# Optimization experiments

Hardware: AMD Instinct MI355X
Metric: run time of the kernel (lower is better)

Reference implementation:

```python
import jax, jax.numpy as jnp
import numpy as np

EPS = 1e-6
K = 16
TEMP = 1.0
RES_SCALE = 0.5
CLAMP_MAX = 50.0


def _knn_indices(x, k):
    # x: (B,N,3) -> idx (B,N,k), self excluded; squared dist preserves ordering
    sq = jnp.sum(x * x, axis=-1)                      # (B,N)
    d2 = sq[:, :, None] + sq[:, None, :] - 2.0 * jnp.einsum('bnd,bmd->bnm', x, x)
    N = x.shape[1]
    eye = jnp.eye(N, dtype=bool)
    d2 = jnp.where(eye[None], jnp.inf, d2)
    _, idx = jax.lax.top_k(-d2, k)
    return idx


def _gather(t, idx):
    # t: (B,N,...), idx: (B,N,k) -> (B,N,k,...)
    return jax.vmap(lambda tb, ib: tb[ib])(t, idx)


def _vn_linear(v, W):
    return jnp.einsum('bncd,oc->bnod', v, W)


def _edge_mlp(s, W1, b1, W2, b2, W3, b3):
    h = jax.nn.silu(s @ W1.T + b1)
    h = jax.nn.silu(h @ W2.T + b2)
    return h @ W3.T + b3


def _vn_layer_norm(x, gamma, beta):
    norm = jnp.maximum(jnp.linalg.norm(x, axis=-1), EPS)      # (B,N,C)
    mean = jnp.mean(norm, axis=-1, keepdims=True)
    std = jnp.maximum(jnp.std(norm, axis=-1, keepdims=True, ddof=1), EPS)
    norm_scaled = (norm - mean) / std * gamma + beta
    return x / norm[..., None] * jnp.maximum(norm_scaled[..., None], EPS)


def _clamp_features(x, max_norm):
    n = jnp.maximum(jnp.linalg.norm(x, axis=-1, keepdims=True), EPS)
    scale = jnp.minimum(max_norm / n, 1.0)
    return x * scale


def setup_inputs() -> dict:
    key = jax.random.key(0)
    ks = jax.random.split(key, 12)
    B, N, C, Cout, H = 8, 2048, 128, 128, 32
    gain = 0.5
    lim = gain * np.sqrt(6.0 / (C + Cout))
    inp = {
        'x': jax.random.normal(ks[0], (B, N, 3), jnp.float32),
        'v': jax.random.normal(ks[1], (B, N, C, 3), jnp.float32),
        'Wq': jax.random.uniform(ks[2], (Cout, C), jnp.float32, -lim, lim),
        'Wk': jax.random.uniform(ks[3], (Cout, C), jnp.float32, -lim, lim),
        'Wu': jax.random.uniform(ks[4], (Cout, C), jnp.float32, -lim, lim),
        'W1': jax.random.normal(ks[5], (H, 4), jnp.float32) * 0.3,
        'b1': jnp.zeros((H,), jnp.float32),
        'W2': jax.random.normal(ks[6], (H, H), jnp.float32) * 0.15,
        'b2': jnp.zeros((H,), jnp.float32),
        'W3': jax.random.normal(ks[7], (1, H), jnp.float32) * 0.15,
        'b3': jnp.zeros((1,), jnp.float32),
        'gamma': jnp.ones((Cout,), jnp.float32),
        'beta': jnp.zeros((Cout,), jnp.float32),
    }
    return inp


def reference(x, v, Wq, Wk, Wu, W1, b1, W2, b2, W3, b3, gamma, beta):
    idx = _knn_indices(jax.lax.stop_gradient(x), K)           # (B,N,k)
    x_nbr = _gather(x, idx)                                    # (B,N,k,3)
    Q = _vn_linear(v, Wq)                                      # (B,N,Co,3)
    Kt = _vn_linear(v, Wk)
    U = _vn_linear(v, Wu)
    K_nbr = _gather(Kt, idx)                                   # (B,N,k,Co,3)
    U_nbr = _gather(U, idx)
    qn = jnp.mean(jnp.linalg.norm(Q, axis=-1), axis=-1, keepdims=True)   # (B,N,1)
    kn = jnp.mean(jnp.linalg.norm(Kt, axis=-1), axis=-1, keepdims=True)
    kn_nbr = _gather(kn, idx)                                  # (B,N,k,1)
    dot_nbr = jnp.mean(jnp.sum(Q[:, :, None] * K_nbr, axis=-1), axis=-1, keepdims=True)  # (B,N,k,1)
    dist = jnp.linalg.norm(x[:, :, None] - x_nbr, axis=-1, keepdims=True)                # (B,N,k,1)
    qn_exp = jnp.broadcast_to(qn[:, :, None], kn_nbr.shape)
    edge_s = jnp.concatenate([qn_exp, kn_nbr, dot_nbr, dist], axis=-1)   # (B,N,k,4)
    logits = jnp.clip(_edge_mlp(edge_s, W1, b1, W2, b2, W3, b3) / TEMP, -10.0, 10.0)
    attn = jax.nn.softmax(logits, axis=2)                      # (B,N,k,1)
    msg = jnp.sum(attn[..., None] * U_nbr, axis=2)             # (B,N,Co,3)
    out = Q + RES_SCALE * msg
    out = _vn_layer_norm(out, gamma, beta)
    out = _clamp_features(out, CLAMP_MAX)
    return out
```

## Files before the change

### kernel.cpp

```cpp
#include <hip/hip_runtime.h>
#include <math.h>

#define BB 8
#define NN 2048
#define CC 128
#define KNB 16
#define BN (BB*NN)
#define WPAD 136

#define EMPTYK 0xFFFFFFFFFFFFFFFFULL

typedef __attribute__((ext_vector_type(8))) short short8;
typedef __attribute__((ext_vector_type(4))) float floatx4;
typedef __attribute__((ext_vector_type(4), aligned(4))) float floatx4u;

__device__ __forceinline__ float silu_f(float x) {
  const float e = __builtin_amdgcn_exp2f(-1.442695040888963f * x);
  return x * __builtin_amdgcn_rcpf(1.0f + e);
}
__device__ __forceinline__ float fsqrt(float x) { return __builtin_amdgcn_sqrtf(x); }
__device__ __forceinline__ float frcp(float x)  { return __builtin_amdgcn_rcpf(x); }

__device__ __forceinline__ unsigned long long umin64(unsigned long long a, unsigned long long b) {
  return (b < a) ? b : a;
}

__device__ __forceinline__ unsigned short f2bf(float f) {
  unsigned u = __float_as_uint(f);
  unsigned r = u + 0x7FFFu + ((u >> 16) & 1u);
  return (unsigned short)(r >> 16);
}
__device__ __forceinline__ float bf2f(unsigned short s) {
  return __uint_as_float(((unsigned)s) << 16);
}

__device__ __forceinline__ float dot8(const float* __restrict__ w, const float* __restrict__ h) {
  const float4 a = *(const float4*)w;
  const float4 b = *(const float4*)(w + 4);
  float s = a.x*h[0];
  s = fmaf(a.y, h[1], s); s = fmaf(a.z, h[2], s); s = fmaf(a.w, h[3], s);
  s = fmaf(b.x, h[4], s); s = fmaf(b.y, h[5], s); s = fmaf(b.z, h[6], s);
  s = fmaf(b.w, h[7], s);
  return s;
}

__global__ __launch_bounds__(256) void sq_kernel(const float* __restrict__ x,
                                                 double* __restrict__ sqd,
                                                 float4* __restrict__ x4) {
  const int i = blockIdx.x*256 + threadIdx.x;
  const float f0 = x[i*3+0], f1 = x[i*3+1], f2 = x[i*3+2];
  const double a0 = (double)f0, a1 = (double)f1, a2 = (double)f2;
  sqd[i] = a0*a0 + a1*a1 + a2*a2;
  x4[i] = make_float4(f0, f1, f2, 0.0f);
}

__global__ __launch_bounds__(512) void knn_kernel(const float4* __restrict__ x4,
                                                  const double* __restrict__ sqd,
                                                  int* __restrict__ idx) {
  const int lane = threadIdx.x & 63;
  const int wave = threadIdx.x >> 6;
  const int bn = blockIdx.x * 8 + wave;
  const int b = bn >> 11;
  const int n = bn & (NN - 1);

  const float4* xb4 = x4 + (size_t)b * NN;
  const double* sqb = sqd + (size_t)b * NN;
  const float4 xq = xb4[n];
  const double xn0 = (double)xq.x, xn1 = (double)xq.y, xn2 = (double)xq.z;
  const double sqn = sqb[n];

  unsigned long long t0 = EMPTYK, t1 = EMPTYK, t2 = EMPTYK, t3 = EMPTYK;

  #pragma unroll 16
  for (int i = 0; i < 32; ++i) {
    const int m = i*64 + lane;
    const float4 xm = xb4[m];
    const double a0 = (double)xm.x, a1 = (double)xm.y, a2 = (double)xm.z;
    const double sqm = sqb[m];
    const double dot = xn0*a0 + xn1*a1 + xn2*a2;
    const double d = sqn + sqm - 2.0*dot;
    unsigned long long kk =
        ((unsigned long long)__double_as_longlong(d) & ~2047ULL) | (unsigned long long)m;
    if (m == n) kk = 0x8000000000000000ULL | (unsigned long long)m;
    const bool l3 = kk < t3, l2 = kk < t2, l1 = kk < t1, l0 = kk < t0;
    t3 = l3 ? (l2 ? t2 : kk) : t3;
    t2 = l2 ? (l1 ? t1 : kk) : t2;
    t1 = l1 ? (l0 ? t0 : kk) : t1;
    t0 = l0 ? kk : t0;
  }

  int* op = idx + (size_t)bn * KNB;
  for (int t = 0; t < KNB; ++t) {
    const unsigned h0 = (unsigned)(t0 >> 32);
    const unsigned l0w = (unsigned)t0;
    unsigned hm = h0;
    #pragma unroll
    for (int off = 32; off > 0; off >>= 1) {
      const unsigned o = (unsigned)__shfl_xor((int)hm, off, 64);
      hm = (o < hm) ? o : hm;
    }
    const bool tied = (h0 == hm);
    const unsigned long long bal = __ballot(tied);
    unsigned lm;
    if (__builtin_popcountll(bal) == 1) {
      const int owner = __builtin_ctzll(bal);
      lm = (unsigned)__shfl((int)l0w, owner, 64);
    } else {
      lm = tied ? l0w : 0xFFFFFFFFu;
      #pragma unroll
      for (int off = 32; off > 0; off >>= 1) {
        const unsigned o = (unsigned)__shfl_xor((int)lm, off, 64);
        lm = (o < lm) ? o : lm;
      }
    }
    const unsigned long long g = ((unsigned long long)hm << 32) | (unsigned long long)lm;

    if (lane == 0) op[t] = (int)(lm & 2047u);

    const bool own = tied && (l0w == lm);
    t0 = own ? t1 : t0;
    t1 = own ? t2 : t1;
    t2 = own ? t3 : t2;
    t3 = own ? EMPTYK : t3;

    const bool need = (t0 == EMPTYK);
    if (__any(need)) {
      unsigned long long nm = EMPTYK;
      #pragma unroll 1
      for (int i = 0; i < 32; ++i) {
        const int m = i*64 + lane;
        const float4 xm = xb4[m];
        const double a0 = (double)xm.x, a1 = (double)xm.y, a2 = (double)xm.z;
        const double sqm = sqb[m];
        const double dot = xn0*a0 + xn1*a1 + xn2*a2;
        const double d = sqn + sqm - 2.0*dot;
        unsigned long long kk =
            ((unsigned long long)__double_as_longlong(d) & ~2047ULL) | (unsigned long long)m;
        if (m == n) kk = 0x8000000000000000ULL | (unsigned long long)m;
        const unsigned long long c = (kk > g) ? kk : EMPTYK;
        nm = umin64(nm, c);
      }
      t0 = need ? nm : t0;
    }
  }
}

__global__ __launch_bounds__(256) void wconv_kernel(
    const float* __restrict__ Wq, const float* __restrict__ Wk, const float* __restrict__ Wu,
    unsigned short* __restrict__ Whl)
{
  const int i = blockIdx.x*256 + threadIdx.x;
  const int mat = i >> 14, rem = i & 16383;
  const float* W = (mat == 0) ? Wq : ((mat == 1) ? Wk : Wu);
  const float f = W[rem];
  const unsigned short h = f2bf(f);
  const float r = f - bf2f(h);
  unsigned short* base = Whl + (size_t)mat * 2 * CC * CC;
  base[rem]           = h;
  base[CC*CC + rem]   = f2bf(r);
}

__global__ __launch_bounds__(256, 2) void vn_gemm_mfma(
    const float* __restrict__ v, const unsigned short* __restrict__ Whl,
    float* __restrict__ Q, float* __restrict__ Kt, float* __restrict__ U)
{
  __shared__ short Wh[CC][WPAD];
  __shared__ short Wl[CC][WPAD];

  const int tid  = threadIdx.x;
  const int lane = tid & 63;
  const int wave = tid >> 6;
  const int quad = lane >> 4;
  const int l15  = lane & 15;

  const int m = blockIdx.x*64 + wave*16 + l15;
  const int p = m / 3, d = m - 3*p;
  const float* vb = v + (size_t)p * (CC*3) + d;
  float areg[32];
  #pragma unroll
  for (int kc = 0; kc < 4; ++kc)
    #pragma unroll
    for (int j = 0; j < 8; ++j)
      areg[kc*8+j] = vb[(kc*32 + quad*8 + j)*3];

  short8 ah[4], al[4];
  #pragma unroll
  for (int kc = 0; kc < 4; ++kc)
    #pragma unroll
    for (int j = 0; j < 8; ++j) {
      const float f = areg[kc*8+j];
      unsigned short h = f2bf(f);
      float r = f - bf2f(h);
      ah[kc][j] = (short)h;
      al[kc][j] = (short)f2bf(r);
    }

  const int r0s = blockIdx.x*64 + wave*16 + quad*4;
  int pbase[4];
  #pragma unroll
  for (int reg = 0; reg < 4; ++reg) {
    const int r = r0s + reg;
    const int pp = r / 3;
    pbase[reg] = pp * (CC*3) + (r - 3*pp);
  }
  const int l153 = l15 * 3;

  for (int mat = 0; mat < 3; ++mat) {
    float* __restrict__ Out = (mat == 0) ? Q : ((mat == 1) ? Kt : U);
    const unsigned short* Wg = Whl + (size_t)mat * 2 * CC * CC;

    #pragma unroll
    for (int it = 0; it < 8; ++it) {
      const int i = it*256 + tid;
      const int o = i >> 4, c8 = (i & 15) * 8;
      *(short8*)&Wh[o][c8] = *(const short8*)&Wg[o*CC + c8];
      *(short8*)&Wl[o][c8] = *(const short8*)&Wg[CC*CC + o*CC + c8];
    }
    __syncthreads();

    floatx4 acc[8];
    #pragma unroll
    for (int ct = 0; ct < 8; ++ct) acc[ct] = (floatx4){0.f, 0.f, 0.f, 0.f};

    #pragma unroll
    for (int kc = 0; kc < 4; ++kc) {
      #pragma unroll
      for (int ct = 0; ct < 8; ++ct) {
        const int o = ct*16 + l15;
        const short8 bh = *(const short8*)&Wh[o][kc*32 + quad*8];
        const short8 bl = *(const short8*)&Wl[o][kc*32 + quad*8];
        acc[ct] = __builtin_amdgcn_mfma_f32_16x16x32_bf16(ah[kc], bh, acc[ct], 0, 0, 0);
        acc[ct] = __builtin_amdgcn_mfma_f32_16x16x32_bf16(al[kc], bh, acc[ct], 0, 0, 0);
        acc[ct] = __builtin_amdgcn_mfma_f32_16x16x32_bf16(ah[kc], bl, acc[ct], 0, 0, 0);
      }
    }
    __syncthreads();

    #pragma unroll
    for (int ct = 0; ct < 8; ++ct) {
      const int o3 = ct*48 + l153;
      #pragma unroll
      for (int reg = 0; reg < 4; ++reg)
        Out[pbase[reg] + o3] = acc[ct][reg];
    }
  }
}

__global__ __launch_bounds__(512) void attn_logits_kernel(
    const float* __restrict__ x, const int* __restrict__ idx,
    const float* __restrict__ Q, const float* __restrict__ Kt,
    const float* __restrict__ W1, const float* __restrict__ b1,
    const float* __restrict__ W2, const float* __restrict__ b2,
    const float* __restrict__ W3, const float* __restrict__ b3,
    float* __restrict__ warr)
{
  __shared__ __align__(16) float W2s[32][32];
  __shared__ __align__(16) float W1s[32][4];
  __shared__ __align__(16) float b1s[32];
  __shared__ __align__(16) float b2s[32];
  __shared__ __align__(16) float W3s[32];
  __shared__ float b3s;

  const int tid  = threadIdx.x;
  const int lane = tid & 63;
  const int wv   = tid >> 6;
  const int bn = ((blockIdx.x & 7) << 11) | ((blockIdx.x >> 3) * 8 + wv);
  const int b = bn >> 11;

  const float* Qp = Q + (size_t)bn * (CC*3) + lane*6;
  const floatx4u q0 = *(const floatx4u*)Qp;
  const float2 q1 = *(const float2*)(Qp+4);

  const int* ip = idx + (size_t)bn * KNB;
  int j[KNB];
  #pragma unroll
  for (int t = 0; t < KNB; ++t) j[t] = ip[t];

  ((float*)W2s)[tid]       = W2[tid];
  ((float*)W2s)[tid + 512] = W2[tid + 512];
  if (tid < 128) ((float*)W1s)[tid] = W1[tid];
  if (tid < 32) { b1s[tid] = b1[tid]; b2s[tid] = b2[tid]; W3s[tid] = W3[tid]; }
  if (tid == 0) b3s = b3[0];
  __syncthreads();

  const float2 qa = make_float2(q0.x, q0.y);
  const float2 qb = make_float2(q0.z, q0.w);
  const float2 qc = make_float2(q1.x, q1.y);

  const int kk = lane & 15;
  int jsel = j[0];
  #pragma unroll
  for (int t = 1; t < KNB; ++t) jsel = (kk == t) ? j[t] : jsel;

  const float xi0 = x[(size_t)bn*3+0], xi1 = x[(size_t)bn*3+1], xi2 = x[(size_t)bn*3+2];
  const float* xj = x + (size_t)(b*NN + jsel)*3;
  const float xj0 = xj[0], xj1 = xj[1], xj2 = xj[2];

  float dpart[KNB], knp[KNB];
  #pragma unroll
  for (int t = 0; t < KNB; ++t) {
    const float* Kp = Kt + (size_t)(b*NN + j[t]) * (CC*3) + lane*6;
    const floatx4u kv = *(const floatx4u*)Kp;
    const float2 kw = *(const float2*)(Kp+4);
    dpart[t] = qa.x*kv.x + qa.y*kv.y + qb.x*kv.z + qb.y*kv.w + qc.x*kw.x + qc.y*kw.y;
    knp[t] = fsqrt(kv.x*kv.x + kv.y*kv.y + kv.z*kv.z) + fsqrt(kv.w*kv.w + kw.x*kw.x + kw.y*kw.y);
  }
  float qnp = fsqrt(qa.x*qa.x + qa.y*qa.y + qb.x*qb.x) + fsqrt(qb.y*qb.y + qc.x*qc.x + qc.y*qc.y);

  #pragma unroll
  for (int off = 1; off < 64; off <<= 1) qnp += __shfl_xor(qnp, off, 64);
  const float s0 = qnp * (1.0f/128.0f);

  float d8[8], k8[8];
  {
    const bool hb = (lane & 1) != 0;
    #pragma unroll
    for (int t = 0; t < 8; ++t) {
      const float dk = hb ? dpart[2*t+1] : dpart[2*t];
      const float dsn = hb ? dpart[2*t]  : dpart[2*t+1];
      const float kv = hb ? knp[2*t+1]   : knp[2*t];
      const float ksn = hb ? knp[2*t]    : knp[2*t+1];
      d8[t] = dk + __shfl_xor(dsn, 1, 64);
      k8[t] = kv + __shfl_xor(ksn, 1, 64);
    }
  }
  float d4[4], k4[4];
  {
    const bool hb = (lane & 2) != 0;
    #pragma unroll
    for (int t = 0; t < 4; ++t) {
      const float dk = hb ? d8[2*t+1] : d8[2*t];
      const float dsn = hb ? d8[2*t]  : d8[2*t+1];
      const float kv = hb ? k8[2*t+1] : k8[2*t];
      const float ksn = hb ? k8[2*t]  : k8[2*t+1];
      d4[t] = dk + __shfl_xor(dsn, 2, 64);
      k4[t] = kv + __shfl_xor(ksn, 2, 64);
    }
  }
  float d2a, d2b, k2a, k2b;
  {
    const bool hb = (lane & 4) != 0;
    const float dk0 = hb ? d4[1] : d4[0];
    const float dsn0 = hb ? d4[0] : d4[1];
    const float dk1 = hb ? d4[3] : d4[2];
    const float dsn1 = hb ? d4[2] : d4[3];
    d2a = dk0 + __shfl_xor(dsn0, 4, 64);
    d2b = dk1 + __shfl_xor(dsn1, 4, 64);
    const float kk0 = hb ? k4[1] : k4[0];
    const float ksn0 = hb ? k4[0] : k4[1];
    const float kk1 = hb ? k4[3] : k4[2];
    const float ksn1 = hb ? k4[2] : k4[3];
    k2a = kk0 + __shfl_xor(ksn0, 4, 64);
    k2b = kk1 + __shfl_xor(ksn1, 4, 64);
  }
  float dsel, knsel;
  {
    const bool hb = (lane & 8) != 0;
    const float dk = hb ? d2b : d2a;
    const float dsn = hb ? d2a : d2b;
    dsel = dk + __shfl_xor(dsn, 8, 64);
    const float kv = hb ? k2b : k2a;
    const float ksn = hb ? k2a : k2b;
    knsel = kv + __shfl_xor(ksn, 8, 64);
  }
  dsel  += __shfl_xor(dsel, 16, 64);
  dsel  += __shfl_xor(dsel, 32, 64);
  knsel += __shfl_xor(knsel, 16, 64);
  knsel += __shfl_xor(knsel, 32, 64);

  const float dx = xi0 - xj0, dy = xi1 - xj1, dz = xi2 - xj2;
  const float s3 = fsqrt(dx*dx + dy*dy + dz*dz);
  const float s1 = knsel * (1.0f/128.0f);
  const float s2 = dsel * (1.0f/128.0f);

  const int g = lane >> 4;
  const int o0 = g*8, o1 = (g^1)*8, o2 = (g^2)*8, o3 = (g^3)*8;

  float h1o[8];
  {
    const float4 b1a = *(const float4*)&b1s[o0];
    const float4 b1b = *(const float4*)&b1s[o0 + 4];
    const float bb1[8] = {b1a.x,b1a.y,b1a.z,b1a.w,b1b.x,b1b.y,b1b.z,b1b.w};
    #pragma unroll
    for (int jj = 0; jj < 8; ++jj) {
      const float4 w = *(const float4*)&W1s[o0 + jj][0];
      float u = bb1[jj];
      u = fmaf(w.x, s0, u); u = fmaf(w.y, s1, u);
      u = fmaf(w.z, s2, u); u = fmaf(w.w, s3, u);
      h1o[jj] = silu_f(u);
    }
  }
  float hx16[8], hx32[8], hx48[8];
  #pragma unroll
  for (int jj = 0; jj < 8; ++jj) hx16[jj] = __shfl_xor(h1o[jj], 16, 64);
  #pragma unroll
  for (int jj = 0; jj < 8; ++jj) hx32[jj] = __shfl_xor(h1o[jj], 32, 64);
  #pragma unroll
  for (int jj = 0; jj < 8; ++jj) hx48[jj] = __shfl_xor(hx16[jj], 32, 64);

  float logit;
  {
    const float4 b2a = *(const float4*)&b2s[o0];
    const float4 b2b = *(const float4*)&b2s[o0 + 4];
    const float bb2[8] = {b2a.x,b2a.y,b2a.z,b2a.w,b2b.x,b2b.y,b2b.z,b2b.w};
    const float4 w3a = *(const float4*)&W3s[o0];
    const float4 w3b = *(const float4*)&W3s[o0 + 4];
    const float ww3[8] = {w3a.x,w3a.y,w3a.z,w3a.w,w3b.x,w3b.y,w3b.z,w3b.w};
    float lp = 0.f;
    #pragma unroll
    for (int hh = 0; hh < 8; ++hh) {
      const float* wr = &W2s[o0 + hh][0];
      float a = bb2[hh];
      a += dot8(wr + o0, h1o);
      a += dot8(wr + o1, hx16);
      a += dot8(wr + o2, hx32);
      a += dot8(wr + o3, hx48);
      lp = fmaf(ww3[hh], silu_f(a), lp);
    }
    lp += __shfl_xor(lp, 16, 64);
    lp += __shfl_xor(lp, 32, 64);
    logit = lp + b3s;
  }
  logit = fminf(fmaxf(logit, -10.0f), 10.0f);

  float mx = logit;
  #pragma unroll
  for (int off = 8; off > 0; off >>= 1) mx = fmaxf(mx, __shfl_xor(mx, off, 16));
  const float e = __builtin_amdgcn_exp2f(1.442695040888963f * (logit - mx));
  float ssum = e;
  #pragma unroll
  for (int off = 8; off > 0; off >>= 1) ssum += __shfl_xor(ssum, off, 16);
  const float w = e * frcp(ssum);

  if (lane < KNB) warr[(size_t)bn * KNB + lane] = w;
}

__global__ __launch_bounds__(512) void attn_msg_kernel(
    const int* __restrict__ idx, const float* __restrict__ Q,
    const float* __restrict__ U, const float* __restrict__ warr,
    const float* __restrict__ gam, const float* __restrict__ bet,
    float* __restrict__ out)
{
  const int lane = threadIdx.x & 63;
  const int wv   = threadIdx.x >> 6;
  const int bn = ((blockIdx.x & 7) << 11) | ((blockIdx.x >> 3) * 8 + wv);
  const int b = bn >> 11;

  const int* ip = idx + (size_t)bn * KNB;
  int j[KNB];
  #pragma unroll
  for (int t = 0; t < KNB; ++t) j[t] = ip[t];

  const float* Qp = Q + (size_t)bn * (CC*3) + lane*6;
  const floatx4u q0 = *(const floatx4u*)Qp;
  const float2 q1 = *(const float2*)(Qp+4);

  const float* wp = warr + (size_t)bn * KNB;
  float wk[KNB];
  #pragma unroll
  for (int t = 0; t < KNB; ++t) wk[t] = wp[t];

  float m0=0.f,m1=0.f,m2=0.f,m3=0.f,m4=0.f,m5=0.f;
  #pragma unroll
  for (int t = 0; t < KNB; ++t) {
    const float* Up = U + (size_t)(b*NN + j[t]) * (CC*3) + lane*6;
    const floatx4u uv = *(const floatx4u*)Up;
    const float2 uw = *(const float2*)(Up+4);
    const float ww = wk[t];
    m0 = fmaf(ww, uv.x, m0); m1 = fmaf(ww, uv.y, m1); m2 = fmaf(ww, uv.z, m2);
    m3 = fmaf(ww, uv.w, m3); m4 = fmaf(ww, uw.x, m4); m5 = fmaf(ww, uw.y, m5);
  }
  const float oa0 = q0.x + 0.5f*m0, oa1 = q0.y + 0.5f*m1, oa2 = q0.z + 0.5f*m2;
  const float ob0 = q0.w + 0.5f*m3, ob1 = q1.x + 0.5f*m4, ob2 = q1.y + 0.5f*m5;

  const float na = fmaxf(fsqrt(oa0*oa0 + oa1*oa1 + oa2*oa2), 1e-6f);
  const float nb = fmaxf(fsqrt(ob0*ob0 + ob1*ob1 + ob2*ob2), 1e-6f);
  float s = na + nb;
  #pragma unroll
  for (int off = 1; off < 64; off <<= 1) s += __shfl_xor(s, off, 64);
  const float mean = s * (1.0f/128.0f);
  const float dva = na - mean, dvb = nb - mean;
  float s2v = dva*dva + dvb*dvb;
  #pragma unroll
  for (int off = 1; off < 64; off <<= 1) s2v += __shfl_xor(s2v, off, 64);
  const float stdv = fmaxf(fsqrt(s2v * (1.0f/127.0f)), 1e-6f);
  const float rstd = frcp(stdv);

  const float2 gm = *(const float2*)(gam + lane*2);
  const float2 bt = *(const float2*)(bet + lane*2);
  const float nsa = (na - mean) * rstd * gm.x + bt.x;
  const float nsb = (nb - mean) * rstd * gm.y + bt.y;
  const float sca = fmaxf(nsa, 1e-6f) * frcp(na);
  const float scb = fmaxf(nsb, 1e-6f) * frcp(nb);
  float fa0 = oa0*sca, fa1 = oa1*sca, fa2 = oa2*sca;
  float fb0 = ob0*scb, fb1 = ob1*scb, fb2 = ob2*scb;
  const float n2a = fmaxf(fsqrt(fa0*fa0 + fa1*fa1 + fa2*fa2), 1e-6f);
  const float n2b = fmaxf(fsqrt(fb0*fb0 + fb1*fb1 + fb2*fb2), 1e-6f);
  const float c2a = fminf(50.0f * frcp(n2a), 1.0f);
  const float c2b = fminf(50.0f * frcp(n2b), 1.0f);

  float* op = out + (size_t)bn * (CC*3) + lane*6;
  floatx4u o4; o4.x = fa0*c2a; o4.y = fa1*c2a; o4.z = fa2*c2a; o4.w = fb0*c2b;
  *(floatx4u*)op = o4;
  *(float2*)(op+4) = make_float2(fb1*c2b, fb2*c2b);
}

extern "C" void kernel_launch(void* const* d_in, const int* in_sizes, int n_in,
                              void* d_out, int out_size, void* d_ws, size_t ws_size,
                              hipStream_t stream) {
  (void)in_sizes; (void)n_in; (void)out_size; (void)ws_size;
  const float* x   = (const float*)d_in[0];
  const float* v   = (const float*)d_in[1];
  const float* Wq  = (const float*)d_in[2];
  const float* Wk  = (const float*)d_in[3];
  const float* Wu  = (const float*)d_in[4];
  const float* W1  = (const float*)d_in[5];
  const float* b1  = (const float*)d_in[6];
  const float* W2  = (const float*)d_in[7];
  const float* b2  = (const float*)d_in[8];
  const float* W3  = (const float*)d_in[9];
  const float* b3  = (const float*)d_in[10];
  const float* gam = (const float*)d_in[11];
  const float* bet = (const float*)d_in[12];
  float* out = (float*)d_out;

  char* ws = (char*)d_ws;
  int*   idx = (int*)ws;
  float* Q   = (float*)(ws + (size_t)BN * KNB * 4);
  float* Kt  = Q  + (size_t)BN * CC * 3;
  float* U   = Kt + (size_t)BN * CC * 3;
  unsigned short* Whl = (unsigned short*)(U + (size_t)BN * CC * 3);
  float* warr = (float*)((char*)Whl + (size_t)3 * 2 * CC * CC * 2);
  double* sqd = (double*)(warr + (size_t)BN * KNB);
  float4* x4  = (float4*)(sqd + (size_t)BN);

  sq_kernel<<<BN/256, 256, 0, stream>>>(x, sqd, x4);
  knn_kernel<<<BN/8, 512, 0, stream>>>(x4, sqd, idx);
  wconv_kernel<<<192, 256, 0, stream>>>(Wq, Wk, Wu, Whl);
  vn_gemm_mfma<<<(BN*3)/64, 256, 0, stream>>>(v, Whl, Q, Kt, U);
  attn_logits_kernel<<<BN/8, 512, 0, stream>>>(x, idx, Q, Kt,
                                               W1, b1, W2, b2, W3, b3, warr);
  attn_msg_kernel<<<BN/8, 512, 0, stream>>>(idx, Q, U, warr, gam, bet, out);
}
```

Baseline: 252.5 us.

## Stage VN GEMM outputs through LDS for coalesced stores; pack kNN coords as doubles

The VN GEMM kernel now runs 6 waves (96 rows, 32 points) per block and writes each accumulator tile to shared memory, then copies it out with contiguous float4 stores instead of scattered stride-3 scalar stores. The shared buffer is reused for the weight tiles, which adds two extra barriers per matrix. Separately, the kNN preprocessing stores x and its squared norm as four doubles per point, so the kNN inner loop does two 16-byte loads and no float-to-double conversions. In exchange the kNN loop reads twice as many bytes per point, and the GEMM block shape and occupancy hint change.

Result: slower. 270.2 us (+7.0%).

```diff
diff --git a/kernel.cpp b/kernel.cpp
--- a/kernel.cpp
+++ b/kernel.cpp
@@ -44,18 +44,17 @@
   return s;
 }
 
-__global__ __launch_bounds__(256) void sq_kernel(const float* __restrict__ x,
-                                                 double* __restrict__ sqd,
-                                                 float4* __restrict__ x4) {
+__global__ __launch_bounds__(256) void xd_kernel(const float* __restrict__ x,
+                                                 double* __restrict__ xd) {
   const int i = blockIdx.x*256 + threadIdx.x;
-  const float f0 = x[i*3+0], f1 = x[i*3+1], f2 = x[i*3+2];
-  const double a0 = (double)f0, a1 = (double)f1, a2 = (double)f2;
-  sqd[i] = a0*a0 + a1*a1 + a2*a2;
-  x4[i] = make_float4(f0, f1, f2, 0.0f);
-}
-
-__global__ __launch_bounds__(512) void knn_kernel(const float4* __restrict__ x4,
-                                                  const double* __restrict__ sqd,
+  const double a0 = (double)x[i*3+0], a1 = (double)x[i*3+1], a2 = (double)x[i*3+2];
+  double2 p0; p0.x = a0; p0.y = a1;
+  double2 p1; p1.x = a2; p1.y = a0*a0 + a1*a1 + a2*a2;
+  *(double2*)&xd[(size_t)i*4]     = p0;
+  *(double2*)&xd[(size_t)i*4 + 2] = p1;
+}
+
+__global__ __launch_bounds__(512) void knn_kernel(const double* __restrict__ xd,
                                                   int* __restrict__ idx) {
   const int lane = threadIdx.x & 63;
   const int wave = threadIdx.x >> 6;
@@ -63,22 +62,21 @@
   const int b = bn >> 11;
   const int n = bn & (NN - 1);
 
-  const float4* xb4 = x4 + (size_t)b * NN;
-  const double* sqb = sqd + (size_t)b * NN;
-  const float4 xq = xb4[n];
-  const double xn0 = (double)xq.x, xn1 = (double)xq.y, xn2 = (double)xq.z;
-  const double sqn = sqb[n];
+  const double* xdb = xd + (size_t)b * NN * 4;
+  const double2 q0 = *(const double2*)&xdb[(size_t)n*4];
+  const double2 q1 = *(const double2*)&xdb[(size_t)n*4 + 2];
+  const double xn0 = q0.x, xn1 = q0.y, xn2 = q1.x;
+  const double sqn = q1.y;
 
   unsigned long long t0 = EMPTYK, t1 = EMPTYK, t2 = EMPTYK, t3 = EMPTYK;
 
   #pragma unroll 16
   for (int i = 0; i < 32; ++i) {
     const int m = i*64 + lane;
-    const float4 xm = xb4[m];
-    const double a0 = (double)xm.x, a1 = (double)xm.y, a2 = (double)xm.z;
-    const double sqm = sqb[m];
-    const double dot = xn0*a0 + xn1*a1 + xn2*a2;
-    const double d = sqn + sqm - 2.0*dot;
+    const double2 p0 = *(const double2*)&xdb[(size_t)m*4];
+    const double2 p1 = *(const double2*)&xdb[(size_t)m*4 + 2];
+    const double dot = xn0*p0.x + xn1*p0.y + xn2*p1.x;
+    const double d = sqn + p1.y - 2.0*dot;
     unsigned long long kk =
         ((unsigned long long)__double_as_longlong(d) & ~2047ULL) | (unsigned long long)m;
     if (m == n) kk = 0x8000000000000000ULL | (unsigned long long)m;
@@ -129,11 +127,10 @@
       #pragma unroll 1
       for (int i = 0; i < 32; ++i) {
         const int m = i*64 + lane;
-        const float4 xm = xb4[m];
-        const double a0 = (double)xm.x, a1 = (double)xm.y, a2 = (double)xm.z;
-        const double sqm = sqb[m];
-        const double dot = xn0*a0 + xn1*a1 + xn2*a2;
-        const double d = sqn + sqm - 2.0*dot;
+        const double2 p0 = *(const double2*)&xdb[(size_t)m*4];
+        const double2 p1 = *(const double2*)&xdb[(size_t)m*4 + 2];
+        const double dot = xn0*p0.x + xn1*p0.y + xn2*p1.x;
+        const double d = sqn + p1.y - 2.0*dot;
         unsigned long long kk =
             ((unsigned long long)__double_as_longlong(d) & ~2047ULL) | (unsigned long long)m;
         if (m == n) kk = 0x8000000000000000ULL | (unsigned long long)m;
@@ -160,12 +157,14 @@
   base[CC*CC + rem]   = f2bf(r);
 }
 
-__global__ __launch_bounds__(256, 2) void vn_gemm_mfma(
+__global__ __launch_bounds__(384, 3) void vn_gemm_mfma(
     const float* __restrict__ v, const unsigned short* __restrict__ Whl,
     float* __restrict__ Q, float* __restrict__ Kt, float* __restrict__ U)
 {
-  __shared__ short Wh[CC][WPAD];
-  __shared__ short Wl[CC][WPAD];
+  __shared__ __align__(16) char smem[69632];
+  short (*Wh)[WPAD] = (short (*)[WPAD])smem;
+  short (*Wl)[WPAD] = (short (*)[WPAD])(smem + (size_t)CC * WPAD * 2);
+  float* ldsT = (float*)smem;
 
   const int tid  = threadIdx.x;
   const int lane = tid & 63;
@@ -173,7 +172,7 @@
   const int quad = lane >> 4;
   const int l15  = lane & 15;
 
-  const int m = blockIdx.x*64 + wave*16 + l15;
+  const int m = blockIdx.x*96 + wave*16 + l15;
   const int p = m / 3, d = m - 3*p;
   const float* vb = v + (size_t)p * (CC*3) + d;
   float areg[32];
@@ -195,26 +194,27 @@
       al[kc][j] = (short)f2bf(r);
     }
 
-  const int r0s = blockIdx.x*64 + wave*16 + quad*4;
-  int pbase[4];
+  int loff[4];
   #pragma unroll
   for (int reg = 0; reg < 4; ++reg) {
-    const int r = r0s + reg;
-    const int pp = r / 3;
-    pbase[reg] = pp * (CC*3) + (r - 3*pp);
-  }
-  const int l153 = l15 * 3;
+    const int rl = wave*16 + quad*4 + reg;
+    const int ppl = rl / 3;
+    loff[reg] = ppl*384 + (rl - 3*ppl);
+  }
+  const size_t gbase = (size_t)blockIdx.x * 12288;
 
   for (int mat = 0; mat < 3; ++mat) {
     float* __restrict__ Out = (mat == 0) ? Q : ((mat == 1) ? Kt : U);
     const unsigned short* Wg = Whl + (size_t)mat * 2 * CC * CC;
 
     #pragma unroll
-    for (int it = 0; it < 8; ++it) {
-      const int i = it*256 + tid;
-      const int o = i >> 4, c8 = (i & 15) * 8;
-      *(short8*)&Wh[o][c8] = *(const short8*)&Wg[o*CC + c8];
-      *(short8*)&Wl[o][c8] = *(const short8*)&Wg[CC*CC + o*CC + c8];
+    for (int it = 0; it < 6; ++it) {
+      const int i = it*384 + tid;
+      if (i < 2048) {
+        const int o = i >> 4, c8 = (i & 15) * 8;
+        *(short8*)&Wh[o][c8] = *(const short8*)&Wg[o*CC + c8];
+        *(short8*)&Wl[o][c8] = *(const short8*)&Wg[CC*CC + o*CC + c8];
+      }
     }
     __syncthreads();
 
@@ -238,11 +238,19 @@
 
     #pragma unroll
     for (int ct = 0; ct < 8; ++ct) {
-      const int o3 = ct*48 + l153;
+      const int o3 = (ct*16 + l15) * 3;
       #pragma unroll
       for (int reg = 0; reg < 4; ++reg)
-        Out[pbase[reg] + o3] = acc[ct][reg];
-    }
+        ldsT[loff[reg] + o3] = acc[ct][reg];
+    }
+    __syncthreads();
+
+    #pragma unroll
+    for (int k = 0; k < 8; ++k) {
+      const int fo = (k*384 + tid) * 4;
+      *(float4*)&Out[gbase + fo] = *(const float4*)&ldsT[fo];
+    }
+    __syncthreads();
   }
 }
 
@@ -531,13 +539,12 @@
   float* U   = Kt + (size_t)BN * CC * 3;
   unsigned short* Whl = (unsigned short*)(U + (size_t)BN * CC * 3);
   float* warr = (float*)((char*)Whl + (size_t)3 * 2 * CC * CC * 2);
-  double* sqd = (double*)(warr + (size_t)BN * KNB);
-  float4* x4  = (float4*)(sqd + (size_t)BN);
-
-  sq_kernel<<<BN/256, 256, 0, stream>>>(x, sqd, x4);
-  knn_kernel<<<BN/8, 512, 0, stream>>>(x4, sqd, idx);
+  double* xd  = (double*)(warr + (size_t)BN * KNB);
+
+  xd_kernel<<<BN/256, 256, 0, stream>>>(x, xd);
+  knn_kernel<<<BN/8, 512, 0, stream>>>(xd, idx);
   wconv_kernel<<<192, 256, 0, stream>>>(Wq, Wk, Wu, Whl);
-  vn_gemm_mfma<<<(BN*3)/64, 256, 0, stream>>>(v, Whl, Q, Kt, U);
+  vn_gemm_mfma<<<(BN*3)/96, 384, 0, stream>>>(v, Whl, Q, Kt, U);
   attn_logits_kernel<<<BN/8, 512, 0, stream>>>(x, idx, Q, Kt,
                                                W1, b1, W2, b2, W3, b3, warr);
   attn_msg_kernel<<<BN/8, 512, 0, stream>>>(idx, Q, U, warr, gam, bet, out);
```

## Stage VN GEMM outputs through LDS for coalesced float4 stores, 6 waves per block

Applied to the files above, without the earlier changes.

The VN linear GEMM now stages each output tile in shared memory (reusing the weight buffers) and writes it back with contiguous float4 stores, replacing the earlier strided scalar stores. Blocks grow to 384 threads covering 96 rows, which is 32 points, so each block's output is one contiguous 12288-float chunk. The cost is two extra barriers per matrix and an LDS transpose, plus changed occupancy from the larger block and shared-memory footprint.

Result: no change. 254.0 us (+0.6%).

```diff
diff --git a/kernel.cpp b/kernel.cpp
--- a/kernel.cpp
+++ b/kernel.cpp
@@ -160,12 +160,14 @@
   base[CC*CC + rem]   = f2bf(r);
 }
 
-__global__ __launch_bounds__(256, 2) void vn_gemm_mfma(
+__global__ __launch_bounds__(384, 3) void vn_gemm_mfma(
     const float* __restrict__ v, const unsigned short* __restrict__ Whl,
     float* __restrict__ Q, float* __restrict__ Kt, float* __restrict__ U)
 {
-  __shared__ short Wh[CC][WPAD];
-  __shared__ short Wl[CC][WPAD];
+  __shared__ __align__(16) char smem[69632];
+  short (*Wh)[WPAD] = (short (*)[WPAD])smem;
+  short (*Wl)[WPAD] = (short (*)[WPAD])(smem + (size_t)CC * WPAD * 2);
+  float* ldsT = (float*)smem;
 
   const int tid  = threadIdx.x;
   const int lane = tid & 63;
@@ -173,7 +175,7 @@
   const int quad = lane >> 4;
   const int l15  = lane & 15;
 
-  const int m = blockIdx.x*64 + wave*16 + l15;
+  const int m = blockIdx.x*96 + wave*16 + l15;
   const int p = m / 3, d = m - 3*p;
   const float* vb = v + (size_t)p * (CC*3) + d;
   float areg[32];
@@ -195,26 +197,27 @@
       al[kc][j] = (short)f2bf(r);
     }
 
-  const int r0s = blockIdx.x*64 + wave*16 + quad*4;
-  int pbase[4];
+  int loff[4];
   #pragma unroll
   for (int reg = 0; reg < 4; ++reg) {
-    const int r = r0s + reg;
-    const int pp = r / 3;
-    pbase[reg] = pp * (CC*3) + (r - 3*pp);
-  }
-  const int l153 = l15 * 3;
+    const int rl = wave*16 + quad*4 + reg;
+    const int ppl = rl / 3;
+    loff[reg] = ppl*384 + (rl - 3*ppl);
+  }
+  const size_t gbase = (size_t)blockIdx.x * 12288;
 
   for (int mat = 0; mat < 3; ++mat) {
     float* __restrict__ Out = (mat == 0) ? Q : ((mat == 1) ? Kt : U);
     const unsigned short* Wg = Whl + (size_t)mat * 2 * CC * CC;
 
     #pragma unroll
-    for (int it = 0; it < 8; ++it) {
-      const int i = it*256 + tid;
-      const int o = i >> 4, c8 = (i & 15) * 8;
-      *(short8*)&Wh[o][c8] = *(const short8*)&Wg[o*CC + c8];
-      *(short8*)&Wl[o][c8] = *(const short8*)&Wg[CC*CC + o*CC + c8];
+    for (int it = 0; it < 6; ++it) {
+      const int i = it*384 + tid;
+      if (i < 2048) {
+        const int o = i >> 4, c8 = (i & 15) * 8;
+        *(short8*)&Wh[o][c8] = *(const short8*)&Wg[o*CC + c8];
+        *(short8*)&Wl[o][c8] = *(const short8*)&Wg[CC*CC + o*CC + c8];
+      }
     }
     __syncthreads();
 
@@ -238,11 +241,19 @@
 
     #pragma unroll
     for (int ct = 0; ct < 8; ++ct) {
-      const int o3 = ct*48 + l153;
+      const int o3 = (ct*16 + l15) * 3;
       #pragma unroll
       for (int reg = 0; reg < 4; ++reg)
-        Out[pbase[reg] + o3] = acc[ct][reg];
-    }
+        ldsT[loff[reg] + o3] = acc[ct][reg];
+    }
+    __syncthreads();
+
+    #pragma unroll
+    for (int k = 0; k < 8; ++k) {
+      const int fo = (k*384 + tid) * 4;
+      *(float4*)&Out[gbase + fo] = *(const float4*)&ldsT[fo];
+    }
+    __syncthreads();
   }
 }
 
@@ -537,7 +548,7 @@
   sq_kernel<<<BN/256, 256, 0, stream>>>(x, sqd, x4);
   knn_kernel<<<BN/8, 512, 0, stream>>>(x4, sqd, idx);
   wconv_kernel<<<192, 256, 0, stream>>>(Wq, Wk, Wu, Whl);
-  vn_gemm_mfma<<<(BN*3)/64, 256, 0, stream>>>(v, Whl, Q, Kt, U);
+  vn_gemm_mfma<<<(BN*3)/96, 384, 0, stream>>>(v, Whl, Q, Kt, U);
   attn_logits_kernel<<<BN/8, 512, 0, stream>>>(x, idx, Q, Kt,
                                                W1, b1, W2, b2, W3, b3, warr);
   attn_msg_kernel<<<BN/8, 512, 0, stream>>>(idx, Q, U, warr, gam, bet, out);
```
